# Kernel tuning notes

Measured on AMD Instinct MI355X. Metric: run time of the kernel, lower is better.

## Reference

```python
import jax, jax.numpy as jnp
import numpy as np

NUM_LAYERS = 3


def setup_inputs() -> dict:
    key = jax.random.key(0)
    ks = jax.random.split(key, 12)
    N, E, D_IN, D, ED = 50000, 800000, 6, 64, 4
    return {
        "x": jax.random.normal(ks[0], (N, D_IN), dtype=jnp.float32),
        "edge_index": jax.random.randint(ks[1], (2, E), 0, N, dtype=jnp.int64),
        "edge_attr": jax.random.normal(ks[2], (E, ED), dtype=jnp.float32),
        "z_soft": jax.random.uniform(ks[3], (E, ED), dtype=jnp.float32),
        "W_nt": jax.random.normal(ks[4], (D, D_IN), dtype=jnp.float32) * 0.1,
        "b_nt": jax.random.normal(ks[5], (D,), dtype=jnp.float32) * 0.1,
        "weight": jax.random.normal(ks[6], (NUM_LAYERS, D, D), dtype=jnp.float32) * 0.1,
        "W_ih": jax.random.normal(ks[7], (3 * D, D), dtype=jnp.float32) * 0.1,
        "W_hh": jax.random.normal(ks[8], (3 * D, D), dtype=jnp.float32) * 0.1,
        "b_ih": jax.random.normal(ks[9], (3 * D,), dtype=jnp.float32) * 0.1,
        "b_hh": jax.random.normal(ks[10], (3 * D,), dtype=jnp.float32) * 0.1,
    }


def gru_cell(m, h, W_ih, W_hh, b_ih, b_hh):
    # PyTorch GRUCell: gates ordered (r, z, n)
    gi = m @ W_ih.T + b_ih
    gh = h @ W_hh.T + b_hh
    i_r, i_z, i_n = jnp.split(gi, 3, axis=-1)
    h_r, h_z, h_n = jnp.split(gh, 3, axis=-1)
    r = jax.nn.sigmoid(i_r + h_r)
    z = jax.nn.sigmoid(i_z + h_z)
    n = jnp.tanh(i_n + r * h_n)
    return (1.0 - z) * n + z * h


def reference(x, edge_index, edge_attr, z_soft, W_nt, b_nt, weight, W_ih, W_hh, b_ih, b_hh):
    # node_transform: Linear + ReLU
    h = jax.nn.relu(x @ W_nt.T + b_nt)  # [N, D]
    # edge_attr gating (faithful to source; unused since edge_weight=None)
    _ = z_soft * edge_attr
    src, dst = edge_index[0], edge_index[1]
    N = h.shape[0]
    for i in range(NUM_LAYERS):
        m = h @ weight[i]                                   # [N, D]
        agg = jax.ops.segment_sum(m[src], dst, num_segments=N)  # gather-scatter add
        h = gru_cell(agg, h, W_ih, W_hh, b_ih, b_hh)
    return h
```

## Files before the change

### kernel.cpp

```cpp
#include <hip/hip_runtime.h>
#include <hip/hip_bf16.h>
#include <stdint.h>

#define D 64
typedef __hip_bfloat16 bf16;
typedef unsigned short u16;
typedef __attribute__((ext_vector_type(8))) short bf16x8;
typedef __attribute__((ext_vector_type(4))) float f32x4;

#define OVF_CAP 65536

__device__ __forceinline__ float bf2f(u16 u) { return __uint_as_float(((uint32_t)u) << 16); }
__device__ __forceinline__ u16 f2bf(float f) { return __bfloat16_as_ushort(__float2bfloat16(f)); }

template <bool F32>
__device__ __forceinline__ float ld(const void* p, int i) {
    if constexpr (F32) return ((const float*)p)[i];
    else return bf2f(((const u16*)p)[i]);
}

__global__ __launch_bounds__(256) void detect_kernel(const void* x, const int* ei, int* flags) {
    __shared__ float smax[256];
    __shared__ int sor[256];
    int t = threadIdx.x;
    const u16* xs = (const u16*)x;
    float mx = 0.f;
#pragma unroll
    for (int i = 0; i < 16; ++i) {
        float a = fabsf(bf2f(xs[t * 16 + i]));
        if (!(a == a)) a = 1e30f;
        mx = fmaxf(mx, a);
    }
    int any = 0;
#pragma unroll
    for (int i = 0; i < 8; ++i) any |= ei[2 * (t * 8 + i) + 1];
    smax[t] = mx; sor[t] = any;
    __syncthreads();
    for (int s = 128; s > 0; s >>= 1) {
        if (t < s) { smax[t] = fmaxf(smax[t], smax[t + s]); sor[t] |= sor[t + s]; }
        __syncthreads();
    }
    if (t == 0) { flags[0] = (smax[0] > 1000.f) ? 1 : 0; flags[1] = (sor[0] != 0) ? 1 : 0; }
}

__global__ __launch_bounds__(256) void convert_edges(const int* __restrict__ flags,
                                                     const int* __restrict__ ei,
                                                     uint32_t* __restrict__ pe, int E, int N) {
    int i0 = blockIdx.x * 1024 + threadIdx.x;
    bool i32 = flags[1] != 0;
#pragma unroll
    for (int u = 0; u < 4; ++u) {
        int i = i0 + u * 256;
        if (i < E) {
            int src, dst;
            if (i32) { src = ei[i];     dst = ei[E + i]; }
            else     { src = ei[2 * i]; dst = ei[2 * (E + i)]; }
            uint32_t v;
            if ((unsigned)src >= (unsigned)N || (unsigned)dst >= (unsigned)N) v = 0xFFFFFFFFu;
            else v = (uint32_t)(u16)src | ((uint32_t)dst << 16);
            pe[i] = v;
        }
    }
}

#define N_WCT 36864
#define N_WTH 12288
#define N_B   384
template <bool F32>
__device__ __forceinline__ void nt_body(const void* x, const void* Wnt, const void* bnt,
                                        u16* ht, int N, int blk) {
    int gid = blk * 256 + threadIdx.x;
    if (gid >= N * D) return;
    int n = gid >> 6, c = gid & 63;
    float acc = ld<F32>(bnt, c);
#pragma unroll
    for (int k = 0; k < 6; ++k)
        acc = fmaf(ld<F32>(x, n * 6 + k), ld<F32>(Wnt, c * 6 + k), acc);
    ht[gid] = f2bf(fmaxf(acc, 0.f));
}
template <bool F32>
__device__ __forceinline__ void wc_body(const void* W, const void* Wih, const void* Whh,
                                        const void* bih, const void* bhh,
                                        u16* WCh, u16* WCl, u16* WVh, u16* WVl,
                                        float* B, int blk) {
    int i = blk * 256 + threadIdx.x;
    if (i < N_WCT) {
        int l = i / 12288, rem = i % 12288, k = rem / 192, r = rem % 192;
        float acc = 0.f;
#pragma unroll 8
        for (int j = 0; j < 64; ++j)
            acc = fmaf(ld<F32>(W, l * 4096 + k * 64 + j), ld<F32>(Wih, r * 64 + j), acc);
        u16 hi = f2bf(acc);
        WCh[l * 12288 + r * 64 + k] = hi;
        WCl[l * 12288 + r * 64 + k] = f2bf(acc - bf2f(hi));
    } else if (i < N_WCT + N_WTH) {
        int rem = i - N_WCT;
        int k = rem / 192, r = rem % 192;
        float v = ld<F32>(Whh, r * 64 + k);
        u16 hi = f2bf(v);
        WVh[r * 64 + k] = hi;
        WVl[r * 64 + k] = f2bf(v - bf2f(hi));
    } else if (i < N_WCT + N_WTH + N_B) {
        int rem = i - N_WCT - N_WTH;
        B[rem] = (rem < 192) ? ld<F32>(bih, rem) : ld<F32>(bhh, rem - 192);
    }
}
__global__ __launch_bounds__(256) void prep_all(const int* __restrict__ flags,
                                                const void* x, const void* Wnt, const void* bnt,
                                                const void* W, const void* Wih, const void* Whh,
                                                const void* bih, const void* bhh,
                                                u16* ht, u16* WCh, u16* WCl, u16* WVh, u16* WVl,
                                                float* B,
                                                const uint32_t* __restrict__ pe,
                                                int* __restrict__ cnt,
                                                u16* __restrict__ ss16, int* __restrict__ novf,
                                                int* __restrict__ ovf,
                                                int E, int N, int NT_BLK, int WC_BLK, int EPS) {
    int b = blockIdx.x;
    if (b < NT_BLK) {
        if (flags[0]) nt_body<true>(x, Wnt, bnt, ht, N, b);
        else          nt_body<false>(x, Wnt, bnt, ht, N, b);
    } else if (b < NT_BLK + WC_BLK) {
        if (flags[0]) wc_body<true>(W, Wih, Whh, bih, bhh, WCh, WCl, WVh, WVl, B, b - NT_BLK);
        else          wc_body<false>(W, Wih, Whh, bih, bhh, WCh, WCl, WVh, WVl, B, b - NT_BLK);
    } else {
        int bf = b - NT_BLK - WC_BLK;
        unsigned shard = (unsigned)(b & 7);
        int beg = (bf >> 3) * EPS;
        int end = beg + EPS; if (end > E) end = E;
        for (int i = beg + (int)threadIdx.x; i < end; i += 256) {
            uint32_t e = pe[i];
            int dst = (int)(e >> 16);
            if ((((unsigned)dst >> 4) & 7u) != shard) continue;
            if (dst >= N) continue;
            int src = (int)(e & 0xffffu);
            int pos = atomicAdd(&cnt[dst], 1);
            if (pos < 64) ss16[(size_t)dst * 64 + pos] = (u16)src;
            else {
                int o = atomicAdd(novf, 1);
                if (o < OVF_CAP) { ovf[2 * o] = dst; ovf[2 * o + 1] = src; }
            }
        }
    }
}

#define NPB 16
#define LSTR 68

#define SGATH(P, E0, E1) { \
    int nu_ = n0 + w4 + P; \
    int dgp_ = 0; \
    if (nu_ < N) { \
        dgp_ = cnt[nu_]; if (dgp_ > 64) dgp_ = 64; \
        const uint32_t* bpd_ = (const uint32_t*)(ss16 + (size_t)nu_ * 64); \
        _Pragma("unroll") for (int q_ = 0; q_ < 8; ++q_) { \
            uint32_t wq_ = bpd_[q_]; \
            int ixE_ = (int)(wq_ & 0xffffu); if (ixE_ > N) ixE_ = N; \
            int ixO_ = (int)(wq_ >> 16);     if (ixO_ > N) ixO_ = N; \
            int ix_ = half ? ixO_ : ixE_; \
            uint32_t d_ = htd[(uint32_t)ix_ * 32u + (uint32_t)col]; \
            E0 += __uint_as_float(d_ << 16); \
            E1 += __uint_as_float(d_ & 0xffff0000u); } \
        if (dgp_ > 16) { \
            _Pragma("unroll") for (int q_ = 8; q_ < 16; ++q_) { \
                uint32_t wq_ = bpd_[q_]; \
                int ixE_ = (int)(wq_ & 0xffffu); if (ixE_ > N) ixE_ = N; \
                int ixO_ = (int)(wq_ >> 16);     if (ixO_ > N) ixO_ = N; \
                int ix_ = half ? ixO_ : ixE_; \
                uint32_t d_ = htd[(uint32_t)ix_ * 32u + (uint32_t)col]; \
                E0 += __uint_as_float(d_ << 16); \
                E1 += __uint_as_float(d_ & 0xffff0000u); } } \
    } \
    dgs[P] = dgp_; }

#define GTAIL(P, E0, E1) if (dgs[P] > 32) { \
    const uint32_t* bpd_ = (const uint32_t*)(ss16 + (size_t)(n0 + w4 + P) * 64); \
    for (int j = 32; j < dgs[P]; ++j) { \
        uint32_t wq_ = bpd_[j >> 1]; \
        int ix_ = (j & 1) ? (int)(wq_ >> 16) : (int)(wq_ & 0xffffu); \
        if (ix_ > N) ix_ = N; \
        uint32_t d_ = htd[(uint32_t)ix_ * 32u + (uint32_t)col]; \
        E0 += __uint_as_float(d_ << 16); \
        E1 += __uint_as_float(d_ & 0xffff0000u); } }

__global__ __launch_bounds__(256) void layer_fused(const int* __restrict__ flags,
                                                   const u16* __restrict__ ht,
                                                   const int* __restrict__ cnt,
                                                   const u16* __restrict__ ss16,
                                                   const int* __restrict__ novf,
                                                   const int* __restrict__ ovf,
                                                   const u16* __restrict__ WCh,
                                                   const u16* __restrict__ WCl,
                                                   const u16* __restrict__ WVh,
                                                   const u16* __restrict__ WVl,
                                                   const float* __restrict__ B,
                                                   u16* __restrict__ houtb,
                                                   void* __restrict__ dout,
                                                   int N) {
    __shared__ alignas(16) float LA[NPB * LSTR];
    __shared__ alignas(16) float LH[NPB * LSTR];
    __shared__ alignas(16) u16 Ahi[NPB * 64];
    __shared__ alignas(16) u16 Alo[NPB * 64];
    __shared__ alignas(16) u16 Hb[NPB * 64];
    int t = threadIdx.x;
    int n0 = blockIdx.x * NPB;
    int lane = t & 63;
    int w4 = __builtin_amdgcn_readfirstlane(t >> 6) * 4;
    int wv = w4 >> 2;
    int half = lane >> 5;
    int col = lane & 31;
    const uint32_t* htd = (const uint32_t*)ht;

    {
        if (t < 128) {
            int row = t >> 3, c = (t & 7) * 8;
            bool v = (n0 + row) < N;
            uint4 vh = make_uint4(0u, 0u, 0u, 0u);
            if (v) vh = *(const uint4*)(ht + (size_t)(n0 + row) * D + c);
            float4 f0, f1;
            f0.x = bf2f((u16)(vh.x & 0xffff)); f0.y = bf2f((u16)(vh.x >> 16));
            f0.z = bf2f((u16)(vh.y & 0xffff)); f0.w = bf2f((u16)(vh.y >> 16));
            f1.x = bf2f((u16)(vh.z & 0xffff)); f1.y = bf2f((u16)(vh.z >> 16));
            f1.z = bf2f((u16)(vh.w & 0xffff)); f1.w = bf2f((u16)(vh.w >> 16));
            *(float4*)&LH[row * LSTR + c]     = f0;
            *(float4*)&LH[row * LSTR + c + 4] = f1;
            *(uint4*)((char*)Hb + row * 128 + ((c * 2) ^ ((row & 7) << 4))) = vh;
        }
    }

    int dgs[4];
    float e00 = 0.f, e01 = 0.f, e10 = 0.f, e11 = 0.f;
    float e20 = 0.f, e21 = 0.f, e30 = 0.f, e31 = 0.f;
    SGATH(0, e00, e01) SGATH(1, e10, e11) SGATH(2, e20, e21) SGATH(3, e30, e31)
    e00 += __shfl_xor(e00, 32); e01 += __shfl_xor(e01, 32);
    e10 += __shfl_xor(e10, 32); e11 += __shfl_xor(e11, 32);
    e20 += __shfl_xor(e20, 32); e21 += __shfl_xor(e21, 32);
    e30 += __shfl_xor(e30, 32); e31 += __shfl_xor(e31, 32);
    GTAIL(0, e00, e01) GTAIL(1, e10, e11) GTAIL(2, e20, e21) GTAIL(3, e30, e31)
    if (half == 0) {
        float2 v0 = {e00, e01}, v1 = {e10, e11}, v2 = {e20, e21}, v3 = {e30, e31};
        *(float2*)&LA[(w4 + 0) * LSTR + 2 * col] = v0;
        *(float2*)&LA[(w4 + 1) * LSTR + 2 * col] = v1;
        *(float2*)&LA[(w4 + 2) * LSTR + 2 * col] = v2;
        *(float2*)&LA[(w4 + 3) * LSTR + 2 * col] = v3;
    }
    __syncthreads();
    {
        int nv = novf[0];
        if (nv > 0) {
            if (nv > OVF_CAP) nv = OVF_CAP;
            for (int o = wv; o < nv; o += 4) {
                int dst = ovf[2 * o];
                if (dst >= n0 && dst < n0 + NPB) {
                    int src = ovf[2 * o + 1];
                    atomicAdd(&LA[(dst - n0) * LSTR + lane], bf2f(ht[(size_t)src * D + lane]));
                }
            }
        }
    }
    __syncthreads();
    {
        int row = t >> 4, c = (t & 15) * 4;
        float4 v = *(const float4*)&LA[row * LSTR + c];
        u16 h0 = f2bf(v.x), h1 = f2bf(v.y), h2 = f2bf(v.z), h3 = f2bf(v.w);
        uint2 hh, llv;
        hh.x = (uint32_t)h0 | ((uint32_t)h1 << 16);
        hh.y = (uint32_t)h2 | ((uint32_t)h3 << 16);
        llv.x = (uint32_t)f2bf(v.x - bf2f(h0)) | ((uint32_t)f2bf(v.y - bf2f(h1)) << 16);
        llv.y = (uint32_t)f2bf(v.z - bf2f(h2)) | ((uint32_t)f2bf(v.w - bf2f(h3)) << 16);
        int off = row * 128 + ((c * 2) ^ ((row & 7) << 4));
        *(uint2*)((char*)Ahi + off) = hh;
        *(uint2*)((char*)Alo + off) = llv;
    }
    __syncthreads();

    int r = lane & 15, g = lane >> 4;
    int aoff0 = r * 128 + (((g * 16) + 0) ^ ((r & 7) << 4));
    int aoff1 = r * 128 + (((g * 16) + 64) ^ ((r & 7) << 4));
    bf16x8 aH0 = *(const bf16x8*)((const char*)Ahi + aoff0);
    bf16x8 aH1 = *(const bf16x8*)((const char*)Ahi + aoff1);
    bf16x8 aL0 = *(const bf16x8*)((const char*)Alo + aoff0);
    bf16x8 aL1 = *(const bf16x8*)((const char*)Alo + aoff1);
    bf16x8 hB0 = *(const bf16x8*)((const char*)Hb + aoff0);
    bf16x8 hB1 = *(const bf16x8*)((const char*)Hb + aoff1);

#define WFRAG(P, nt, ks) (*(const bf16x8*)((const char*)(P) + ((nt) * 16 + r) * 128 + (ks) * 64 + g * 16))
#define DO_TILE(nt, ai, ah) { \
    bf16x8 wch0 = WFRAG(WCh, nt, 0), wch1 = WFRAG(WCh, nt, 1); \
    bf16x8 wcl0 = WFRAG(WCl, nt, 0), wcl1 = WFRAG(WCl, nt, 1); \
    bf16x8 wvh0 = WFRAG(WVh, nt, 0), wvh1 = WFRAG(WVh, nt, 1); \
    bf16x8 wvl0 = WFRAG(WVl, nt, 0), wvl1 = WFRAG(WVl, nt, 1); \
    ai = __builtin_amdgcn_mfma_f32_16x16x32_bf16(aH0, wch0, ai, 0, 0, 0); \
    ai = __builtin_amdgcn_mfma_f32_16x16x32_bf16(aH1, wch1, ai, 0, 0, 0); \
    ai = __builtin_amdgcn_mfma_f32_16x16x32_bf16(aL0, wch0, ai, 0, 0, 0); \
    ai = __builtin_amdgcn_mfma_f32_16x16x32_bf16(aL1, wch1, ai, 0, 0, 0); \
    ai = __builtin_amdgcn_mfma_f32_16x16x32_bf16(aH0, wcl0, ai, 0, 0, 0); \
    ai = __builtin_amdgcn_mfma_f32_16x16x32_bf16(aH1, wcl1, ai, 0, 0, 0); \
    ah = __builtin_amdgcn_mfma_f32_16x16x32_bf16(hB0, wvh0, ah, 0, 0, 0); \
    ah = __builtin_amdgcn_mfma_f32_16x16x32_bf16(hB1, wvh1, ah, 0, 0, 0); \
    ah = __builtin_amdgcn_mfma_f32_16x16x32_bf16(hB0, wvl0, ah, 0, 0, 0); \
    ah = __builtin_amdgcn_mfma_f32_16x16x32_bf16(hB1, wvl1, ah, 0, 0, 0); }

    f32x4 air = {0.f, 0.f, 0.f, 0.f}, aiz = air, ain = air;
    f32x4 ahr = air, ahz = air, ahn = air;
    DO_TILE(wv, air, ahr);
    DO_TILE(wv + 4, aiz, ahz);
    DO_TILE(wv + 8, ain, ahn);

    {
        int ch = wv * 16 + r;
        float br = B[ch] + B[192 + ch];
        float bz = B[64 + ch] + B[256 + ch];
        float bi = B[128 + ch];
        float bh = B[320 + ch];
        int nb = g * 4;
#pragma unroll
        for (int j = 0; j < 4; ++j) {
            float gr = air[j] + ahr[j] + br;
            float gz = aiz[j] + ahz[j] + bz;
            float rr = 1.f / (1.f + __expf(-gr));
            float zz = 1.f / (1.f + __expf(-gz));
            float nx = ain[j] + bi + rr * (ahn[j] + bh);
            float th = 1.f - 2.f / (1.f + __expf(2.f * nx));
            float hold = LH[(nb + j) * LSTR + ch];
            LA[(nb + j) * LSTR + ch] = (1.f - zz) * th + zz * hold;
        }
    }
    __syncthreads();
    if (t < 128) {
        int row = t >> 3, c = (t & 7) * 8;
        int n = n0 + row;
        if (n < N) {
            float4 v0 = *(const float4*)&LA[row * LSTR + c];
            float4 v1 = *(const float4*)&LA[row * LSTR + c + 4];
            size_t idx = (size_t)n * D + c;
            if (houtb || !flags[0]) {
                uint4 o;
                o.x = (uint32_t)f2bf(v0.x) | ((uint32_t)f2bf(v0.y) << 16);
                o.y = (uint32_t)f2bf(v0.z) | ((uint32_t)f2bf(v0.w) << 16);
                o.z = (uint32_t)f2bf(v1.x) | ((uint32_t)f2bf(v1.y) << 16);
                o.w = (uint32_t)f2bf(v1.z) | ((uint32_t)f2bf(v1.w) << 16);
                if (houtb) *(uint4*)(houtb + idx) = o;
                else       *(uint4*)((u16*)dout + idx) = o;
            } else {
                *(float4*)((float*)dout + idx)     = v0;
                *(float4*)((float*)dout + idx + 4) = v1;
            }
        }
    }
}

extern "C" void kernel_launch(void* const* d_in, const int* in_sizes, int n_in,
                              void* d_out, int out_size, void* d_ws, size_t ws_size,
                              hipStream_t stream) {
    const void* x   = d_in[0];
    const int*  ei  = (const int*)d_in[1];
    const void* Wnt = d_in[4];
    const void* bnt = d_in[5];
    const void* Wt  = d_in[6];
    const void* Wih = d_in[7];
    const void* Whh = d_in[8];
    const void* bih = d_in[9];
    const void* bhh = d_in[10];

    int N = in_sizes[0] / 6;
    int E = in_sizes[1] / 2;
    int ND = N * D;

    int* flags = (int*)d_ws;
    float* B   = (float*)((char*)d_ws + 256);
    u16* WCh = (u16*)(B + N_B);
    u16* WCl = WCh + N_WCT;
    u16* WVh = WCl + N_WCT;
    u16* WVl = WVh + N_WTH;
    u16* htA = WVl + N_WTH;
    u16* htB = htA + ND + D;
    int* cnt  = (int*)(htB + ND + D);
    int* novf = cnt + N;
    u16* ss16 = (u16*)(novf + 1);
    int* ovf  = (int*)(ss16 + (size_t)N * 64);
    uint32_t* pe = (uint32_t*)(ovf + 2 * (size_t)OVF_CAP);

    int NT_BLK = (ND + 255) / 256;
    int WC_BLK = (N_WCT + N_WTH + N_B + 255) / 256;
    int FS = (E + 1023) / 1024;
    int EPS = (E + FS - 1) / FS;
    int FI_BLK = 8 * FS;
    int CV_BLK = (E + 1023) / 1024;

    hipMemsetAsync(cnt, 0, (size_t)(N + 1) * sizeof(int), stream);
    hipMemsetAsync(ss16, 0xFF, (size_t)N * 128, stream);
    hipMemsetAsync(htA + (size_t)ND, 0, D * sizeof(u16), stream);
    hipMemsetAsync(htB + (size_t)ND, 0, D * sizeof(u16), stream);
    detect_kernel<<<1, 256, 0, stream>>>(x, ei, flags);
    convert_edges<<<CV_BLK, 256, 0, stream>>>(flags, ei, pe, E, N);
    prep_all<<<NT_BLK + WC_BLK + FI_BLK, 256, 0, stream>>>(flags, x, Wnt, bnt, Wt, Wih, Whh,
                                                           bih, bhh, htA, WCh, WCl, WVh, WVl, B,
                                                           pe, cnt, ss16, novf, ovf,
                                                           E, N, NT_BLK, WC_BLK, EPS);

    u16* hcur = htA;
    u16* hnxt = htB;
    for (int layer = 0; layer < 3; ++layer) {
        bool last = (layer == 2);
        layer_fused<<<(N + NPB - 1) / NPB, 256, 0, stream>>>(flags, hcur, cnt, ss16, novf, ovf,
                                                             WCh + layer * 12288, WCl + layer * 12288,
                                                             WVh, WVl, B,
                                                             last ? nullptr : hnxt,
                                                             last ? d_out : nullptr, N);
        u16* t = hcur; hcur = hnxt; hnxt = t;
    }
}
```

Measured before the change: 313.8 us.

## Fold memsets into convert_edges and use nontemporal loads/stores for streaming data

Replaces the four hipMemsetAsync calls with zero/fill loops inside convert_edges. This removes separate launch and memset overhead, and the 256-byte alignment of ss16 supports its vectorized fill. It also marks streaming accesses as nontemporal: edge list reads, adjacency slot writes and reads, and hidden-state output stores. The nontemporal hints may hurt if the adjacency table or hidden state would otherwise stay in cache between the prep and layer kernels.

```diff
diff --git a/kernel.cpp b/kernel.cpp
--- a/kernel.cpp
+++ b/kernel.cpp
@@ -7,6 +7,7 @@
 typedef unsigned short u16;
 typedef __attribute__((ext_vector_type(8))) short bf16x8;
 typedef __attribute__((ext_vector_type(4))) float f32x4;
+typedef __attribute__((ext_vector_type(4))) unsigned int u32x4;
 
 #define OVF_CAP 65536
 
@@ -45,7 +46,17 @@
 
 __global__ __launch_bounds__(256) void convert_edges(const int* __restrict__ flags,
                                                      const int* __restrict__ ei,
-                                                     uint32_t* __restrict__ pe, int E, int N) {
+                                                     uint32_t* __restrict__ pe, int E, int N,
+                                                     int* __restrict__ cnt,
+                                                     u32x4* __restrict__ ss4,
+                                                     uint32_t* __restrict__ dumA,
+                                                     uint32_t* __restrict__ dumB) {
+    int tid = blockIdx.x * 256 + threadIdx.x;
+    int nth = gridDim.x * 256;
+    for (int i = tid; i < N + 1; i += nth) cnt[i] = 0;
+    u32x4 ff = {0xFFFFFFFFu, 0xFFFFFFFFu, 0xFFFFFFFFu, 0xFFFFFFFFu};
+    for (int i = tid; i < N * 8; i += nth) __builtin_nontemporal_store(ff, ss4 + i);
+    if (tid < 32) { dumA[tid] = 0u; dumB[tid] = 0u; }
     int i0 = blockIdx.x * 1024 + threadIdx.x;
     bool i32 = flags[1] != 0;
 #pragma unroll
@@ -129,13 +140,13 @@
         int beg = (bf >> 3) * EPS;
         int end = beg + EPS; if (end > E) end = E;
         for (int i = beg + (int)threadIdx.x; i < end; i += 256) {
-            uint32_t e = pe[i];
+            uint32_t e = __builtin_nontemporal_load(pe + i);
             int dst = (int)(e >> 16);
             if ((((unsigned)dst >> 4) & 7u) != shard) continue;
             if (dst >= N) continue;
             int src = (int)(e & 0xffffu);
             int pos = atomicAdd(&cnt[dst], 1);
-            if (pos < 64) ss16[(size_t)dst * 64 + pos] = (u16)src;
+            if (pos < 64) __builtin_nontemporal_store((u16)src, ss16 + (size_t)dst * 64 + pos);
             else {
                 int o = atomicAdd(novf, 1);
                 if (o < OVF_CAP) { ovf[2 * o] = dst; ovf[2 * o + 1] = src; }
@@ -154,7 +165,7 @@
         dgp_ = cnt[nu_]; if (dgp_ > 64) dgp_ = 64; \
         const uint32_t* bpd_ = (const uint32_t*)(ss16 + (size_t)nu_ * 64); \
         _Pragma("unroll") for (int q_ = 0; q_ < 8; ++q_) { \
-            uint32_t wq_ = bpd_[q_]; \
+            uint32_t wq_ = __builtin_nontemporal_load(bpd_ + q_); \
             int ixE_ = (int)(wq_ & 0xffffu); if (ixE_ > N) ixE_ = N; \
             int ixO_ = (int)(wq_ >> 16);     if (ixO_ > N) ixO_ = N; \
             int ix_ = half ? ixO_ : ixE_; \
@@ -163,7 +174,7 @@
             E1 += __uint_as_float(d_ & 0xffff0000u); } \
         if (dgp_ > 16) { \
             _Pragma("unroll") for (int q_ = 8; q_ < 16; ++q_) { \
-                uint32_t wq_ = bpd_[q_]; \
+                uint32_t wq_ = __builtin_nontemporal_load(bpd_ + q_); \
                 int ixE_ = (int)(wq_ & 0xffffu); if (ixE_ > N) ixE_ = N; \
                 int ixO_ = (int)(wq_ >> 16);     if (ixO_ > N) ixO_ = N; \
                 int ix_ = half ? ixO_ : ixE_; \
@@ -176,7 +187,7 @@
 #define GTAIL(P, E0, E1) if (dgs[P] > 32) { \
     const uint32_t* bpd_ = (const uint32_t*)(ss16 + (size_t)(n0 + w4 + P) * 64); \
     for (int j = 32; j < dgs[P]; ++j) { \
-        uint32_t wq_ = bpd_[j >> 1]; \
+        uint32_t wq_ = __builtin_nontemporal_load(bpd_ + (j >> 1)); \
         int ix_ = (j & 1) ? (int)(wq_ >> 16) : (int)(wq_ & 0xffffu); \
         if (ix_ > N) ix_ = N; \
         uint32_t d_ = htd[(uint32_t)ix_ * 32u + (uint32_t)col]; \
@@ -335,16 +346,18 @@
             float4 v1 = *(const float4*)&LA[row * LSTR + c + 4];
             size_t idx = (size_t)n * D + c;
             if (houtb || !flags[0]) {
-                uint4 o;
+                u32x4 o;
                 o.x = (uint32_t)f2bf(v0.x) | ((uint32_t)f2bf(v0.y) << 16);
                 o.y = (uint32_t)f2bf(v0.z) | ((uint32_t)f2bf(v0.w) << 16);
                 o.z = (uint32_t)f2bf(v1.x) | ((uint32_t)f2bf(v1.y) << 16);
                 o.w = (uint32_t)f2bf(v1.z) | ((uint32_t)f2bf(v1.w) << 16);
-                if (houtb) *(uint4*)(houtb + idx) = o;
-                else       *(uint4*)((u16*)dout + idx) = o;
+                if (houtb) __builtin_nontemporal_store(o, (u32x4*)(houtb + idx));
+                else       __builtin_nontemporal_store(o, (u32x4*)((u16*)dout + idx));
             } else {
-                *(float4*)((float*)dout + idx)     = v0;
-                *(float4*)((float*)dout + idx + 4) = v1;
+                f32x4 w0 = {v0.x, v0.y, v0.z, v0.w};
+                f32x4 w1 = {v1.x, v1.y, v1.z, v1.w};
+                __builtin_nontemporal_store(w0, (f32x4*)((float*)dout + idx));
+                __builtin_nontemporal_store(w1, (f32x4*)((float*)dout + idx + 4));
             }
         }
     }
@@ -377,7 +390,9 @@
     u16* htB = htA + ND + D;
     int* cnt  = (int*)(htB + ND + D);
     int* novf = cnt + N;
-    u16* ss16 = (u16*)(novf + 1);
+    size_t ssoff = (size_t)((char*)(novf + 1) - (char*)d_ws);
+    ssoff = (ssoff + 255) & ~(size_t)255;
+    u16* ss16 = (u16*)((char*)d_ws + ssoff);
     int* ovf  = (int*)(ss16 + (size_t)N * 64);
     uint32_t* pe = (uint32_t*)(ovf + 2 * (size_t)OVF_CAP);
 
@@ -388,12 +403,11 @@
     int FI_BLK = 8 * FS;
     int CV_BLK = (E + 1023) / 1024;
 
-    hipMemsetAsync(cnt, 0, (size_t)(N + 1) * sizeof(int), stream);
-    hipMemsetAsync(ss16, 0xFF, (size_t)N * 128, stream);
-    hipMemsetAsync(htA + (size_t)ND, 0, D * sizeof(u16), stream);
-    hipMemsetAsync(htB + (size_t)ND, 0, D * sizeof(u16), stream);
     detect_kernel<<<1, 256, 0, stream>>>(x, ei, flags);
-    convert_edges<<<CV_BLK, 256, 0, stream>>>(flags, ei, pe, E, N);
+    convert_edges<<<CV_BLK, 256, 0, stream>>>(flags, ei, pe, E, N,
+                                              cnt, (u32x4*)ss16,
+                                              (uint32_t*)(htA + (size_t)ND),
+                                              (uint32_t*)(htB + (size_t)ND));
     prep_all<<<NT_BLK + WC_BLK + FI_BLK, 256, 0, stream>>>(flags, x, Wnt, bnt, Wt, Wih, Whh,
                                                            bih, bhh, htA, WCh, WCl, WVh, WVl, B,
                                                            pe, cnt, ss16, novf, ovf,
```

Result: faster. 300.3 us (-4.3%).
